# Optimization experiments

Hardware: AMD Instinct MI355X
Metric: run time of the kernel (lower is better)

## Reference

```python
import jax, jax.numpy as jnp
import numpy as np

D_MODEL = 2048
NUM_HEADS = 32
NUM_KV_HEADS = 8
D_K = D_MODEL // NUM_HEADS
B, S = 2, 2048


def setup_inputs() -> dict:
    key = jax.random.key(0)
    ks = jax.random.split(key, 6)
    sc = 1.0 / np.sqrt(D_MODEL)
    x = jax.random.normal(ks[0], (B, S, D_MODEL), dtype=jnp.float32)
    mask = jnp.tril(jnp.ones((S, S), dtype=jnp.float32))[None, None]  # [1,1,S,S]
    return {
        'x': x,
        'mask': mask,
        'Wq': jax.random.normal(ks[1], (D_MODEL, D_MODEL), jnp.float32) * sc,
        'bq': jnp.zeros((D_MODEL,), jnp.float32),
        'Wk': jax.random.normal(ks[2], (D_MODEL, NUM_KV_HEADS * D_K), jnp.float32) * sc,
        'bk': jnp.zeros((NUM_KV_HEADS * D_K,), jnp.float32),
        'Wv': jax.random.normal(ks[3], (D_MODEL, NUM_KV_HEADS * D_K), jnp.float32) * sc,
        'bv': jnp.zeros((NUM_KV_HEADS * D_K,), jnp.float32),
        'Wo': jax.random.normal(ks[4], (D_MODEL, D_MODEL), jnp.float32) * sc,
        'bo': jnp.zeros((D_MODEL,), jnp.float32),
    }


def reference(x, mask, Wq, bq, Wk, bk, Wv, bv, Wo, bo):
    b, s, _ = x.shape
    g = NUM_HEADS // NUM_KV_HEADS  # queries per kv head
    Q = (x @ Wq + bq).reshape(b, s, NUM_HEADS, D_K).transpose(0, 2, 1, 3)      # [b,h,s,dk]
    K = (x @ Wk + bk).reshape(b, s, NUM_KV_HEADS, D_K).transpose(0, 2, 1, 3)   # [b,kv,s,dk]
    V = (x @ Wv + bv).reshape(b, s, NUM_KV_HEADS, D_K).transpose(0, 2, 1, 3)
    # group queries per kv head instead of repeat_interleave on K/V
    Qg = Q.reshape(b, NUM_KV_HEADS, g, s, D_K)
    scores = jnp.einsum('bkgqd,bkld->bkgql', Qg, K) / np.sqrt(D_K)             # [b,kv,g,s,s]
    scores = jnp.where(mask[:, :, None] == 0, -1e9, scores)
    attn = jax.nn.softmax(scores, axis=-1)
    out = jnp.einsum('bkgql,bkld->bkgqd', attn, V)                              # [b,kv,g,s,dk]
    out = out.reshape(b, NUM_HEADS, s, D_K).transpose(0, 2, 1, 3).reshape(b, s, D_MODEL)
    return out @ Wo + bo
```

## Files before the change

kernel.cpp:

```cpp
#include <hip/hip_runtime.h>
#include <stdint.h>

typedef __bf16 bf16x8 __attribute__((ext_vector_type(8)));
typedef float  f32x4  __attribute__((ext_vector_type(4)));

__device__ __forceinline__ f32x4 mfma16(bf16x8 a, bf16x8 b, f32x4 c) {
    return __builtin_amdgcn_mfma_f32_16x16x32_bf16(a, b, c, 0, 0, 0);
}

__device__ __forceinline__ uint16_t f2bf(float f) {
    union { __bf16 b; uint16_t u; } cv; cv.b = (__bf16)f; return cv.u;
}

#if __has_builtin(__builtin_amdgcn_exp2f)
#define EXP2F(x) __builtin_amdgcn_exp2f(x)
#else
#define EXP2F(x) __expf((x) * 0.6931471805599453f)
#endif

typedef __attribute__((address_space(3))) void as3_void;
typedef __attribute__((address_space(1))) void as1_void;
__device__ __forceinline__ void async_ld16(const void* g, void* l) {
    __builtin_amdgcn_global_load_lds((const as1_void*)g, (as3_void*)l, 16, 0, 0);
}


__global__ void prep_wx(const float* __restrict__ x,
                        const float* __restrict__ Wq, const float* __restrict__ Wk,
                        const float* __restrict__ Wv, const float* __restrict__ Wo,
                        const float* __restrict__ bq, const float* __restrict__ bk,
                        const float* __restrict__ bv,
                        uint16_t* __restrict__ wqkvT, uint16_t* __restrict__ woT,
                        uint16_t* __restrict__ xb, float* __restrict__ biasq) {
    const int z = blockIdx.z;
    const int tx = threadIdx.x, ty = threadIdx.y;
    if (z == 4) {
        const int tid = ty * 32 + tx;
        const int linear = blockIdx.y * 64 + blockIdx.x;
        const int i = linear * 2048 + tid * 8;
#pragma unroll
        for (int u = 0; u < 2; ++u) {
            float4 v = *(const float4*)(x + i + u * 4);
            ushort4 o;
            o.x = f2bf(v.x); o.y = f2bf(v.y); o.z = f2bf(v.z); o.w = f2bf(v.w);
            *(ushort4*)(xb + i + u * 4) = o;
        }
        if (linear < 12) {
            int bi = linear * 256 + tid;
            biasq[bi] = (bi < 2048) ? bq[bi] : (bi < 2560 ? bk[bi - 2048] : bv[bi - 2560]);
        }
        return;
    }
    __shared__ float tile[32][33];
    const float* in; uint16_t* out; int ldin, off;
    if (z == 0)      { in = Wq; out = wqkvT; ldin = 2048; off = 0; }
    else if (z == 1) { if (blockIdx.x >= 16) return; in = Wk; out = wqkvT; ldin = 512; off = 2048; }
    else if (z == 2) { if (blockIdx.x >= 16) return; in = Wv; out = wqkvT; ldin = 512; off = 2560; }
    else             { in = Wo; out = woT;   ldin = 2048; off = 0; }
    const int c0 = blockIdx.x << 5, r0 = blockIdx.y << 5;
#pragma unroll
    for (int i = 0; i < 4; ++i)
        tile[ty + i * 8][tx] = in[(size_t)(r0 + ty + i * 8) * ldin + c0 + tx];
    __syncthreads();
#pragma unroll
    for (int i = 0; i < 4; ++i)
        out[(size_t)(off + c0 + ty + i * 8) * 2048 + r0 + tx] = f2bf(tile[tx][ty + i * 8]);
}

__global__ void transpose_v(const uint16_t* __restrict__ qkv, uint16_t* __restrict__ vt) {
    __shared__ uint16_t tile[32][33];
    const int c0 = blockIdx.x << 5, r0 = blockIdx.y << 5, b = blockIdx.z;
    const int tx = threadIdx.x, ty = threadIdx.y;
#pragma unroll
    for (int i = 0; i < 4; ++i)
        tile[ty + i * 8][tx] = qkv[(size_t)(b * 2048 + r0 + ty + i * 8) * 3072 + 2560 + c0 + tx];
    __syncthreads();
    const int perm = 4 * (tx >> 3) + (((tx & 7) < 4) ? 0 : 16) + (tx & 3);
#pragma unroll
    for (int i = 0; i < 4; ++i)
        vt[(size_t)(b * 512 + c0 + ty + i * 8) * 2048 + r0 + tx] = tile[perm][ty + i * 8];
}

template <bool F32OUT>
__global__ __launch_bounds__(256, 2)
void gemm_bt(const uint16_t* __restrict__ A, const uint16_t* __restrict__ Bt,
             const float* __restrict__ bias, void* __restrict__ Cout, int N, int K) {
    __shared__ __align__(16) uint16_t As[8192];
    __shared__ __align__(16) uint16_t Bs[8192];
    const int tid = threadIdx.x;
    const int wv = tid >> 6, ln = tid & 63;
    const int quad = ln >> 4, l16 = ln & 15;
    const int row0 = blockIdx.y << 7, col0 = blockIdx.x << 7;
    const int wm = wv >> 1, wn = wv & 1;

    const uint16_t* gA[4];
    const uint16_t* gB[4];
#pragma unroll
    for (int j = 0; j < 4; ++j) {
        int p = j * 256 + tid;
        int r = p >> 3, c = (p & 7) ^ ((r ^ (r >> 3)) & 7);
        gA[j] = A + (size_t)(row0 + r) * K + (c << 3);
        gB[j] = Bt + (size_t)(col0 + r) * K + (c << 3);
    }

    int a_off[4][2], b_off[4][2];
#pragma unroll
    for (int t = 0; t < 4; ++t)
#pragma unroll
        for (int s = 0; s < 2; ++s) {
            int r = (wm << 6) + (t << 4) + l16;
            a_off[t][s] = (((r << 3) + ((4 * s + quad) ^ ((r ^ (r >> 3)) & 7))) << 3);
            r = (wn << 6) + (t << 4) + l16;
            b_off[t][s] = (((r << 3) + ((4 * s + quad) ^ ((r ^ (r >> 3)) & 7))) << 3);
        }

    f32x4 acc[4][4] = {};

    for (int k0 = 0; k0 < K; k0 += 64) {
        __syncthreads();
#pragma unroll
        for (int j = 0; j < 4; ++j) {
            async_ld16(gA[j] + k0, As + (j << 11) + (wv << 9));
            async_ld16(gB[j] + k0, Bs + (j << 11) + (wv << 9));
        }
        __syncthreads();
#pragma unroll
        for (int s = 0; s < 2; ++s) {
            bf16x8 af[4], bfr[4];
#pragma unroll
            for (int t = 0; t < 4; ++t) af[t] = *(const bf16x8*)(As + a_off[t][s]);
#pragma unroll
            for (int t = 0; t < 4; ++t) bfr[t] = *(const bf16x8*)(Bs + b_off[t][s]);
#pragma unroll
            for (int mt = 0; mt < 4; ++mt)
#pragma unroll
                for (int nt = 0; nt < 4; ++nt)
                    acc[mt][nt] = mfma16(af[mt], bfr[nt], acc[mt][nt]);
        }
    }

#pragma unroll
    for (int nt = 0; nt < 4; ++nt) {
        const int col = col0 + (wn << 6) + (nt << 4) + l16;
        const float bv = bias[col];
#pragma unroll
        for (int mt = 0; mt < 4; ++mt) {
            const int rbase = row0 + (wm << 6) + (mt << 4) + (quad << 2);
#pragma unroll
            for (int r = 0; r < 4; ++r) {
                float v = acc[mt][nt][r] + bv;
                if (F32OUT)
                    ((float*)Cout)[(size_t)(rbase + r) * N + col] = v;
                else
                    ((uint16_t*)Cout)[(size_t)(rbase + r) * N + col] = f2bf(v);
            }
        }
    }
}

__global__ __launch_bounds__(256, 2)
void attn_fwd(const uint16_t* __restrict__ QKV, const uint16_t* __restrict__ Vt,
              uint16_t* __restrict__ AO) {
    __shared__ __align__(16) uint16_t smem[32768];
    uint16_t* const Ks = smem;
    uint16_t* const Vs = smem + 16384;

    const int tid = threadIdx.x;
    const int wv = tid >> 6, ln = tid & 63;
    const int quad = ln >> 4, l16 = ln & 15;
    const int p = blockIdx.x, kvh = blockIdx.y, b = blockIdx.z;
    const int h = kvh * 4 + wv;

    const uint16_t* Kg = QKV + (size_t)(b * 2048) * 3072 + 2048 + kvh * 64;
    const uint16_t* Vg = Vt + (size_t)(b * 512 + kvh * 64) * 2048;

    const uint16_t* gK[2];
    const uint16_t* gV[2];
#pragma unroll
    for (int j = 0; j < 2; ++j) {
        int pos = j * 256 + tid;
        int r = pos >> 3, c = (pos & 7) ^ ((r ^ (r >> 3)) & 7);
        gK[j] = Kg + (size_t)r * 3072 + (c << 3);
        gV[j] = Vg + (size_t)r * 2048 + (c << 3);
    }
    const int sdst = wv << 9;

    int kf_off[4][2], vf_off[2][4];
#pragma unroll
    for (int g = 0; g < 4; ++g) {
        int r = g * 16 + l16, gs = (r ^ (r >> 3)) & 7;
#pragma unroll
        for (int kk = 0; kk < 2; ++kk)
            kf_off[g][kk] = ((r << 3) + ((kk * 4 + quad) ^ gs)) << 3;
    }
#pragma unroll
    for (int nt = 0; nt < 4; ++nt) {
        int r = nt * 16 + l16, gs = (r ^ (r >> 3)) & 7;
#pragma unroll
        for (int s = 0; s < 2; ++s)
            vf_off[s][nt] = ((r << 3) + ((s * 4 + quad) ^ gs)) << 3;
    }

#define EXP_PV(MASKED)                                                         \
    _Pragma("unroll")                                                          \
    for (int m = 0; m < 2; ++m) {                                              \
        f32x4 ev[4];                                                           \
        _Pragma("unroll")                                                      \
        for (int g = 0; g < 4; ++g) {                                          \
            f32x4 arg = sv[m][g] * 0.18033688f + (-23.0831207f);               \
            _Pragma("unroll")                                                  \
            for (int rr = 0; rr < 4; ++rr) {                                   \
                float v = EXP2F(arg[rr]);                                      \
                if (MASKED && (16 * g + 4 * quad + rr >                        \
                               32 * wr + 16 * m + l16)) v = 0.0f;              \
                ev[g][rr] = v;                                                 \
            }                                                                  \
        }                                                                      \
        f32x4 s2 = (ev[0] + ev[1]) + (ev[2] + ev[3]);                          \
        lp[m] += (s2[0] + s2[1]) + (s2[2] + s2[3]);                            \
        bf16x8 pf0, pf1;                                                       \
        _Pragma("unroll")                                                      \
        for (int rr = 0; rr < 4; ++rr) {                                       \
            pf0[rr] = (__bf16)ev[0][rr]; pf0[4 + rr] = (__bf16)ev[1][rr];      \
            pf1[rr] = (__bf16)ev[2][rr]; pf1[4 + rr] = (__bf16)ev[3][rr];      \
        }                                                                      \
        __builtin_amdgcn_s_setprio(1);                                         \
        _Pragma("unroll")                                                      \
        for (int nt = 0; nt < 4; ++nt) {                                       \
            acc[m][nt] = mfma16(vf[0][nt], pf0, acc[m][nt]);                   \
            acc[m][nt] = mfma16(vf[1][nt], pf1, acc[m][nt]);                   \
        }                                                                      \
        __builtin_amdgcn_s_setprio(0);                                         \
    }

#define PROC(SUB)                                                              \
    {                                                                          \
        const uint16_t* kb = Ks + (((cur << 1) | SUB) << 12);                  \
        const uint16_t* vb = Vs + (((cur << 1) | SUB) << 12);                  \
        bf16x8 kf[4][2], vf[2][4];                                             \
        _Pragma("unroll")                                                      \
        for (int g = 0; g < 4; ++g)                                            \
            _Pragma("unroll")                                                  \
            for (int kk = 0; kk < 2; ++kk)                                     \
                kf[g][kk] = *(const bf16x8*)(kb + kf_off[g][kk]);              \
        _Pragma("unroll")                                                      \
        for (int s = 0; s < 2; ++s)                                            \
            _Pragma("unroll")                                                  \
            for (int nt = 0; nt < 4; ++nt)                                     \
                vf[s][nt] = *(const bf16x8*)(vb + vf_off[s][nt]);              \
        f32x4 sv[2][4];                                                        \
        __builtin_amdgcn_s_setprio(1);                                         \
        _Pragma("unroll")                                                      \
        for (int m = 0; m < 2; ++m)                                            \
            _Pragma("unroll")                                                  \
            for (int g = 0; g < 4; ++g) {                                      \
                f32x4 z = {0.f, 0.f, 0.f, 0.f};                                \
                z = mfma16(kf[g][0], qf[m][0], z);                             \
                z = mfma16(kf[g][1], qf[m][1], z);                             \
                sv[m][g] = z;                                                  \
            }                                                                  \
        __builtin_amdgcn_s_setprio(0);                                         \
        if ((tw << 1) + SUB == nkb - 1) { EXP_PV(true) }                       \
        else                            { EXP_PV(false) }                      \
    }

#pragma unroll
    for (int half = 0; half < 2; ++half) {
        const int w = half ? (63 - p) : p;
        const int q0 = w << 5;
        const int nkb = (w >> 1) + 1;
        const int nwin = (nkb + 1) >> 1;
        const int wr = w & 1;

        bf16x8 qf[2][2];
#pragma unroll
        for (int m = 0; m < 2; ++m)
#pragma unroll
            for (int kk = 0; kk < 2; ++kk)
                qf[m][kk] = *(const bf16x8*)(QKV +
                    (size_t)(b * 2048 + q0 + m * 16 + l16) * 3072 + h * 64 + kk * 32 + quad * 8);

        f32x4 acc[2][4] = {};
        float lp[2] = {0.0f, 0.0f};

        __syncthreads();
#pragma unroll
        for (int sub = 0; sub < 2; ++sub)
#pragma unroll
            for (int j = 0; j < 2; ++j) {
                async_ld16(gK[j] + (size_t)(sub << 6) * 3072, Ks + (sub << 12) + (j << 11) + sdst);
                async_ld16(gV[j] + (sub << 6),                Vs + (sub << 12) + (j << 11) + sdst);
            }

        for (int tw = 0; tw < nwin; ++tw) {
            const int cur = tw & 1;
            __syncthreads();
            if (tw + 1 < nwin) {
#pragma unroll
                for (int sub = 0; sub < 2; ++sub) {
                    const int tn = ((tw + 1) << 1) + sub;
                    const size_t ko = (size_t)(tn << 6) * 3072;
                    const int vo = tn << 6;
#pragma unroll
                    for (int j = 0; j < 2; ++j) {
                        async_ld16(gK[j] + ko,
                                   Ks + ((((cur ^ 1) << 1) | sub) << 12) + (j << 11) + sdst);
                        async_ld16(gV[j] + vo,
                                   Vs + ((((cur ^ 1) << 1) | sub) << 12) + (j << 11) + sdst);
                    }
                }
            }

            PROC(0)
            if ((tw << 1) + 1 < nkb) PROC(1)
        }

        float inv[2];
#pragma unroll
        for (int m = 0; m < 2; ++m) {
            float rs = lp[m];
            rs += __shfl_xor(rs, 16, 64);
            rs += __shfl_xor(rs, 32, 64);
            inv[m] = 1.0f / rs;
        }

        __syncthreads();
        uint16_t* ot = smem + wv * 2176;
#pragma unroll
        for (int m = 0; m < 2; ++m)
#pragma unroll
            for (int nt = 0; nt < 4; ++nt)
#pragma unroll
                for (int pp = 0; pp < 2; ++pp) {
                    uint32_t pk = (uint32_t)f2bf(acc[m][nt][2 * pp] * inv[m]) |
                                  ((uint32_t)f2bf(acc[m][nt][2 * pp + 1] * inv[m]) << 16);
                    *(uint32_t*)(ot + (m * 16 + l16) * 68 + nt * 16 + quad * 4 + 2 * pp) = pk;
                }
        const int orow = ln >> 1, ohalf = (ln & 1) << 5;
        uint16_t* aobase = AO + (size_t)(b * 2048 + q0 + orow) * 2048 + h * 64 + ohalf;
        const uint16_t* osrc = ot + orow * 68 + ohalf;
#pragma unroll
        for (int c4 = 0; c4 < 4; ++c4)
            *(uint4*)(aobase + c4 * 8) = *(const uint4*)(osrc + c4 * 8);
    }
#undef PROC
#undef EXP_PV
}


extern "C" void kernel_launch(void* const* d_in, const int* in_sizes, int n_in,
                              void* d_out, int out_size, void* d_ws, size_t ws_size,
                              hipStream_t stream) {
    (void)in_sizes; (void)n_in; (void)out_size; (void)ws_size;
    const float* x  = (const float*)d_in[0];
    const float* Wq = (const float*)d_in[2];
    const float* bq = (const float*)d_in[3];
    const float* Wk = (const float*)d_in[4];
    const float* bk = (const float*)d_in[5];
    const float* Wv = (const float*)d_in[6];
    const float* bv = (const float*)d_in[7];
    const float* Wo = (const float*)d_in[8];
    const float* bo = (const float*)d_in[9];

    char* ws = (char*)d_ws;
    uint16_t* xb    = (uint16_t*)ws;
    uint16_t* wqkvT = (uint16_t*)(ws + 16777216);
    uint16_t* woT   = (uint16_t*)(ws + 16777216 + 12582912);
    float*    biasq = (float*)(ws + 16777216 + 12582912 + 8388608);
    uint16_t* qkv   = (uint16_t*)d_out;
    uint16_t* ao    = xb;
    uint16_t* vt    = wqkvT;

    dim3 tb(32, 8);
    prep_wx<<<dim3(64, 64, 5), tb, 0, stream>>>(x, Wq, Wk, Wv, Wo, bq, bk, bv,
                                                wqkvT, woT, xb, biasq);
    gemm_bt<false><<<dim3(24, 32), 256, 0, stream>>>(xb, wqkvT, biasq, qkv, 3072, 2048);
    transpose_v<<<dim3(16, 64, 2), tb, 0, stream>>>(qkv, vt);
    attn_fwd<<<dim3(32, 8, 2), 256, 0, stream>>>(qkv, vt, ao);
    gemm_bt<true><<<dim3(16, 32), 256, 0, stream>>>(ao, woT, bo, d_out, 2048, 2048);
}
```

Measured before the change: 285.6 us.

## Double-buffer GEMM LDS tiles with async prefetch two stages ahead

Converts the projection GEMM main loop from single-buffered to a two-stage LDS ping-pong, issuing async global-to-LDS loads for tile kt+2 while MFMAs run on the current tile. It adds explicit vmcnt/lgkmcnt waits, raw s_barriers, sched_barriers and s_setprio around the MFMA block. The goal is to hide global load latency behind compute. The cost is doubled LDS use (64KB per block), which may lower occupancy below the two blocks per CU the launch bounds request.

```diff
diff --git a/kernel.cpp b/kernel.cpp
--- a/kernel.cpp
+++ b/kernel.cpp
@@ -85,8 +85,8 @@
 __global__ __launch_bounds__(256, 2)
 void gemm_bt(const uint16_t* __restrict__ A, const uint16_t* __restrict__ Bt,
              const float* __restrict__ bias, void* __restrict__ Cout, int N, int K) {
-    __shared__ __align__(16) uint16_t As[8192];
-    __shared__ __align__(16) uint16_t Bs[8192];
+    __shared__ __align__(16) uint16_t As[2][8192];
+    __shared__ __align__(16) uint16_t Bs[2][8192];
     const int tid = threadIdx.x;
     const int wv = tid >> 6, ln = tid & 63;
     const int quad = ln >> 4, l16 = ln & 15;
@@ -116,39 +116,61 @@
 
     f32x4 acc[4][4] = {};
 
-    for (int k0 = 0; k0 < K; k0 += 64) {
-        __syncthreads();
-#pragma unroll
-        for (int j = 0; j < 4; ++j) {
-            async_ld16(gA[j] + k0, As + (j << 11) + (wv << 9));
-            async_ld16(gB[j] + k0, Bs + (j << 11) + (wv << 9));
-        }
-        __syncthreads();
-#pragma unroll
-        for (int s = 0; s < 2; ++s) {
-            bf16x8 af[4], bfr[4];
-#pragma unroll
-            for (int t = 0; t < 4; ++t) af[t] = *(const bf16x8*)(As + a_off[t][s]);
-#pragma unroll
-            for (int t = 0; t < 4; ++t) bfr[t] = *(const bf16x8*)(Bs + b_off[t][s]);
+#define STAGE(T, D)                                                            \
+    _Pragma("unroll")                                                          \
+    for (int j = 0; j < 4; ++j) {                                              \
+        async_ld16(gA[j] + ((T) << 6), As[D] + (j << 11) + (wv << 9));         \
+        async_ld16(gB[j] + ((T) << 6), Bs[D] + (j << 11) + (wv << 9));         \
+    }
+
+    const int NT = K >> 6;
+    STAGE(0, 0)
+    STAGE(1, 1)
+
+    for (int kt = 0; kt < NT; ++kt) {
+        const int d = kt & 1;
+        if (kt < NT - 1) asm volatile("s_waitcnt vmcnt(8)" ::: "memory");
+        else             asm volatile("s_waitcnt vmcnt(0)" ::: "memory");
+        __builtin_amdgcn_s_barrier();
+        __builtin_amdgcn_sched_barrier(0);
+
+        bf16x8 af[2][4], bfr[2][4];
+#pragma unroll
+        for (int s = 0; s < 2; ++s)
+#pragma unroll
+            for (int t = 0; t < 4; ++t) {
+                af[s][t]  = *(const bf16x8*)(As[d] + a_off[t][s]);
+                bfr[s][t] = *(const bf16x8*)(Bs[d] + b_off[t][s]);
+            }
+        asm volatile("s_waitcnt lgkmcnt(0)" ::: "memory");
+        __builtin_amdgcn_sched_barrier(0);
+        __builtin_amdgcn_s_barrier();
+        __builtin_amdgcn_sched_barrier(0);
+
+        if (kt + 2 < NT) STAGE(kt + 2, d)
+
+        __builtin_amdgcn_s_setprio(1);
+#pragma unroll
+        for (int s = 0; s < 2; ++s)
 #pragma unroll
             for (int mt = 0; mt < 4; ++mt)
 #pragma unroll
-                for (int nt = 0; nt < 4; ++nt)
-                    acc[mt][nt] = mfma16(af[mt], bfr[nt], acc[mt][nt]);
-        }
-    }
-
-#pragma unroll
-    for (int nt = 0; nt < 4; ++nt) {
-        const int col = col0 + (wn << 6) + (nt << 4) + l16;
+                for (int nn = 0; nn < 4; ++nn)
+                    acc[mt][nn] = mfma16(af[s][mt], bfr[s][nn], acc[mt][nn]);
+        __builtin_amdgcn_s_setprio(0);
+    }
+#undef STAGE
+
+#pragma unroll
+    for (int nn = 0; nn < 4; ++nn) {
+        const int col = col0 + (wn << 6) + (nn << 4) + l16;
         const float bv = bias[col];
 #pragma unroll
         for (int mt = 0; mt < 4; ++mt) {
             const int rbase = row0 + (wm << 6) + (mt << 4) + (quad << 2);
 #pragma unroll
             for (int r = 0; r < 4; ++r) {
-                float v = acc[mt][nt][r] + bv;
+                float v = acc[mt][nn][r] + bv;
                 if (F32OUT)
                     ((float*)Cout)[(size_t)(rbase + r) * N + col] = v;
                 else
```

Result: no change. 288.8 us (+1.1%).
